# Optimization experiments

Measured on AMD Instinct MI355X. Metric: run time of the kernel, lower is better.

## Reference

```python
import jax, jax.numpy as jnp
import numpy as np

B = 32768
SEQ_LEN = 24
H = 64            # HIDDEN_DIM
SLOTS = 8         # MEMORY_SLOTS
VOCAB = 64        # VOCAB_SIZE


def setup_inputs() -> dict:
    key = jax.random.key(0)
    ks = jax.random.split(key, 8)
    seqs = jax.random.randint(ks[0], (B, SEQ_LEN), 0, VOCAB, dtype=jnp.int64)
    query_tok = jax.random.randint(ks[1], (B,), 0, VOCAB + 2, dtype=jnp.int64)
    embed = jax.random.normal(ks[2], (VOCAB + 2, H), dtype=jnp.float32) * 0.05
    gw1 = jax.random.normal(ks[3], (2 * H, 32), dtype=jnp.float32) / np.sqrt(2 * H)
    gb1 = jnp.zeros((32,), jnp.float32)
    gw2 = jax.random.normal(ks[4], (32, 1), dtype=jnp.float32) / np.sqrt(32)
    gb2 = jnp.zeros((1,), jnp.float32)
    rw1 = jax.random.normal(ks[5], (2 * H, H), dtype=jnp.float32) / np.sqrt(2 * H)
    rb1 = jnp.zeros((H,), jnp.float32)
    rw2 = jax.random.normal(ks[6], (H, VOCAB), dtype=jnp.float32) / np.sqrt(H)
    rb2 = jnp.zeros((VOCAB,), jnp.float32)
    return {"seqs": seqs, "query_tok": query_tok, "embed": embed,
            "gw1": gw1, "gb1": gb1, "gw2": gw2, "gb2": gb2,
            "rw1": rw1, "rb1": rb1, "rw2": rw2, "rb2": rb2}


def reference(seqs, query_tok, embed, gw1, gb1, gw2, gb2, rw1, rb1, rw2, rb2):
    Bb = seqs.shape[0]
    T = SEQ_LEN - 1  # model writes tokens 0..SEQ_LEN-2 into memory
    embs = embed[seqs[:, :T]]                     # [B, T, H]
    batch_idx = jnp.arange(Bb)

    def step(mem, xs):
        t, emb = xs                               # emb: [B, H]
        ctx = jnp.broadcast_to(emb[:, None, :], mem.shape)
        pair = jnp.concatenate([ctx, mem], axis=-1)        # [B, S, 2H]
        h = jax.nn.relu(pair @ gw1 + gb1)                  # [B, S, 32]
        score = jax.nn.sigmoid(h @ gw2 + gb2)[..., 0]      # [B, S]
        # while memory not full, fill slot t; otherwise evict argmax score
        idx = jnp.where(t < SLOTS, t, jnp.argmax(score, axis=1))
        mem = mem.at[batch_idx, idx].set(emb)
        return mem, None

    mem0 = jnp.zeros((Bb, SLOTS, H), embed.dtype)
    mem, _ = jax.lax.scan(step, mem0, (jnp.arange(T), jnp.swapaxes(embs, 0, 1)))

    summary = mem.mean(axis=1)                    # [B, H]  (memory is full: T > SLOTS)
    q = embed[query_tok]                          # [B, H]
    x = jnp.concatenate([q, summary], axis=-1)    # [B, 2H]
    logits = jax.nn.relu(x @ rw1 + rb1) @ rw2 + rb2   # [B, VOCAB]
    return logits
```

## Files before the change

kernel.cpp:

```cpp
#include <hip/hip_runtime.h>
#include <math.h>

typedef __attribute__((ext_vector_type(8))) _Float16 f16x8;
typedef __attribute__((ext_vector_type(4))) float f32x4;

#define TSTEPS 23

#define WSB_Z  0
#define WSB_B1 16384
#define WSB_W2 37888

__global__ __launch_bounds__(256) void pre_all(
    const float* __restrict__ embed, const float* __restrict__ gw1,
    const float* __restrict__ gb1, const float* __restrict__ gw2,
    const float* __restrict__ gb2, const float* __restrict__ rw1,
    const float* __restrict__ rb1, const float* __restrict__ rw2,
    char* __restrict__ wsc)
{
    __shared__ float sEmb[66 * 64];
    __shared__ float sW[128 * 64];
    __shared__ float sV[64 * 33];
    __shared__ float sU[4 * 32];
    __shared__ float sG[65];
    __shared__ float sRb1[64];

    const int tid = threadIdx.x;
    const int blk = blockIdx.x;

    if (blk < 16) {
        {
            const float4* es = (const float4*)embed;
            float4* ed = (float4*)sEmb;
            for (int i = tid; i < 1024; i += 256) ed[i] = es[i];
            const float4* gs = (const float4*)gw1;
            float4* gd = (float4*)sW;
            for (int i = tid; i < 1024; i += 256) gd[i] = gs[i];
            if (tid < 32) { sG[tid] = gb1[tid]; sG[32 + tid] = gw2[tid]; }
            if (tid == 64) sG[64] = gb2[0];
        }
        __syncthreads();
        #pragma unroll
        for (int i = 0; i < 8; ++i) {
            const int e = tid + i * 256;
            const int s = e >> 5, j = e & 31;
            float acc = 0.f;
            const float* er = sEmb + s * 64;
            #pragma unroll
            for (int k = 0; k < 64; ++k)
                acc = fmaf(er[k], sW[(64 + k) * 32 + j], acc);
            sV[s * 33 + j] = acc;
        }
        if (tid < 128) {
            const int cc = tid >> 5, j = tid & 31;
            const int c = blk * 4 + cc;
            float acc = 0.f;
            const float* er = sEmb + c * 64;
            #pragma unroll
            for (int k = 0; k < 64; ++k)
                acc = fmaf(er[k], sW[k * 32 + j], acc);
            sU[cc * 32 + j] = acc;
        }
        __syncthreads();
        const int cc = tid >> 6, s = tid & 63;
        const int c = blk * 4 + cc;
        double z = (double)sG[64];
        #pragma unroll
        for (int j = 0; j < 32; ++j) {
            const double a = (double)sU[cc * 32 + j] + (double)sV[s * 33 + j] + (double)sG[j];
            if (a > 0.0) z += a * (double)sG[32 + j];
        }
        ((float*)(wsc + WSB_Z))[c * 64 + s] = (float)(1.0 / (1.0 + exp(-z)));
    } else if (blk < 49) {
        {
            const float4* es = (const float4*)embed;
            float4* ed = (float4*)sEmb;
            for (int i = tid; i < 1056; i += 256) ed[i] = es[i];
            const float4* rs = (const float4*)rw1;
            float4* rd = (float4*)sW;
            for (int i = tid; i < 2048; i += 256) rd[i] = rs[i];
            if (tid < 64) sRb1[tid] = rb1[tid];
        }
        __syncthreads();
        const int e = (blk - 16) * 256 + tid;
        if (e < 8320) {
            const int n = e & 63, k = e >> 6;
            float acc;
            if (k < 64) {
                acc = 0.f;
                const float* er = sEmb + k * 64;
                #pragma unroll
                for (int m = 0; m < 64; ++m)
                    acc = fmaf(er[m], sW[(64 + m) * 64 + n], acc);
                acc *= 0.125f * 256.f;
            } else {
                const int t = k - 64;
                acc = sRb1[n];
                const float* er = sEmb + t * 64;
                #pragma unroll
                for (int m = 0; m < 64; ++m)
                    acc = fmaf(er[m], sW[m * 64 + n], acc);
                acc *= 256.f;
            }
            ((_Float16*)(wsc + WSB_B1))[n * 168 + k] = (_Float16)acc;
        }
    } else {
        _Float16* w2t = (_Float16*)(wsc + WSB_W2);
        for (int e = tid; e < 4096; e += 256) {
            const int n = e & 63, j = e >> 6;
            w2t[n * 72 + j] = (_Float16)rw2[j * 64 + n];
        }
        _Float16* b1 = (_Float16*)(wsc + WSB_B1);
        for (int e = tid; e < 2432; e += 256) {
            const int n = e / 38, k = 130 + (e - n * 38);
            b1[n * 168 + k] = (_Float16)0.f;
        }
    }
}

#define ROWS 128

__global__ __launch_bounds__(512, 2) void sm_main(
    const int* __restrict__ seqs, const int* __restrict__ qtok,
    const float* __restrict__ rb2, const char* __restrict__ wsc,
    float* __restrict__ out)
{
    __shared__ __align__(16) float     sZ[64 * 64];
    __shared__ __align__(16) _Float16  sB1[64 * 168];
    __shared__ __align__(16) _Float16  sA[128 * 168];
    __shared__ __align__(16) _Float16  sW2[64 * 72];
    __shared__ __align__(16) _Float16  sH[128 * 72];
    __shared__ float sRb2[64];

    const int tid = threadIdx.x;
    const int base = blockIdx.x * ROWS;

    unsigned pk[6];
    int qt = 0;
    if (tid < ROWS) {
        const int4* sq = (const int4*)(seqs + (size_t)(base + tid) * 24);
        #pragma unroll
        for (int i = 0; i < 6; ++i) {
            const int4 w4 = sq[i];
            pk[i] = (unsigned)w4.x | ((unsigned)w4.y << 8) |
                    ((unsigned)w4.z << 16) | ((unsigned)w4.w << 24);
        }
        qt = qtok[base + tid];
    }

    {
        const float4* zsrc = (const float4*)(wsc + WSB_Z);
        float4* zdst = (float4*)sZ;
        for (int i = tid; i < 1024; i += 512) zdst[i] = zsrc[i];
        const float4* b1s = (const float4*)(wsc + WSB_B1);
        float4* b1d = (float4*)sB1;
        for (int i = tid; i < 1344; i += 512) b1d[i] = b1s[i];
        const float4* w2s = (const float4*)(wsc + WSB_W2);
        float4* w2d = (float4*)sW2;
        for (int i = tid; i < 576; i += 512) w2d[i] = w2s[i];
        const float4 z4 = {0.f, 0.f, 0.f, 0.f};
        float4* ad = (float4*)sA;
        for (int i = tid; i < 2688; i += 512) ad[i] = z4;
        if (tid < 64) sRb2[tid] = rb2[tid];
    }
    __syncthreads();

    if (tid < ROWS) {
        unsigned lo = pk[0], hi = pk[1];
        #pragma unroll
        for (int t = 8; t < TSTEPS; ++t) {
            const int c = (int)((pk[t >> 2] >> ((t & 3) * 8)) & 255u);
            const float* zr = sZ + c * 64;
            float b = zr[lo & 63]; int am = 0; float z;
            z = zr[(lo >> 8) & 63];  if (z > b) { b = z; am = 1; }
            z = zr[(lo >> 16) & 63]; if (z > b) { b = z; am = 2; }
            z = zr[lo >> 24];        if (z > b) { b = z; am = 3; }
            z = zr[hi & 63];         if (z > b) { b = z; am = 4; }
            z = zr[(hi >> 8) & 63];  if (z > b) { b = z; am = 5; }
            z = zr[(hi >> 16) & 63]; if (z > b) { b = z; am = 6; }
            z = zr[hi >> 24];        if (z > b) { b = z; am = 7; }
            const unsigned cb = (unsigned)c;
            if (am < 4) { const int sh = am * 8; lo = (lo & ~(255u << sh)) | (cb << sh); }
            else        { const int sh = am * 8 - 32; hi = (hi & ~(255u << sh)) | (cb << sh); }
        }
        int t_[8] = { (int)(lo & 63), (int)((lo >> 8) & 63), (int)((lo >> 16) & 63), (int)(lo >> 24),
                      (int)(hi & 63), (int)((hi >> 8) & 63), (int)((hi >> 16) & 63), (int)(hi >> 24) };
        int tot[8] = {1, 1, 1, 1, 1, 1, 1, 1};
        #pragma unroll
        for (int i = 0; i < 8; ++i)
            #pragma unroll
            for (int j = i + 1; j < 8; ++j) {
                const int eq = (t_[i] == t_[j]);
                tot[i] += eq; tot[j] += eq;
            }
        _Float16* arow = sA + tid * 168;
        #pragma unroll
        for (int i = 0; i < 8; ++i) arow[t_[i]] = (_Float16)(float)tot[i];
        arow[64 + qt] = (_Float16)1.0f;
    }
    __syncthreads();

    const int lane = tid & 63;
    const int w = tid >> 6;
    const int c16 = lane & 15, g = lane >> 4;
    const int arow = w * 16 + c16;
    f32x4 a0 = {0.f, 0.f, 0.f, 0.f}, a1 = a0, a2 = a0, a3 = a0;
    #pragma unroll
    for (int ks = 0; ks < 5; ++ks) {
        const int ko = ks * 32 + g * 8;
        const f16x8 af = *(const f16x8*)&sA[arow * 168 + ko];
        const f16x8 b0 = *(const f16x8*)&sB1[(c16) * 168 + ko];
        const f16x8 b1 = *(const f16x8*)&sB1[(16 + c16) * 168 + ko];
        const f16x8 b2 = *(const f16x8*)&sB1[(32 + c16) * 168 + ko];
        const f16x8 b3 = *(const f16x8*)&sB1[(48 + c16) * 168 + ko];
        a0 = __builtin_amdgcn_mfma_f32_16x16x32_f16(af, b0, a0, 0, 0, 0);
        a1 = __builtin_amdgcn_mfma_f32_16x16x32_f16(af, b1, a1, 0, 0, 0);
        a2 = __builtin_amdgcn_mfma_f32_16x16x32_f16(af, b2, a2, 0, 0, 0);
        a3 = __builtin_amdgcn_mfma_f32_16x16x32_f16(af, b3, a3, 0, 0, 0);
    }
    {
        const int rbase = w * 16 + g * 4;
        #pragma unroll
        for (int j = 0; j < 4; ++j) {
            _Float16* hr = sH + (rbase + j) * 72;
            const float v0 = a0[j], v1 = a1[j], v2 = a2[j], v3 = a3[j];
            hr[c16]      = (_Float16)(v0 > 0.f ? v0 : 0.f);
            hr[16 + c16] = (_Float16)(v1 > 0.f ? v1 : 0.f);
            hr[32 + c16] = (_Float16)(v2 > 0.f ? v2 : 0.f);
            hr[48 + c16] = (_Float16)(v3 > 0.f ? v3 : 0.f);
        }
    }
    __syncthreads();

    f32x4 d0 = {0.f, 0.f, 0.f, 0.f}, d1 = d0, d2 = d0, d3 = d0;
    #pragma unroll
    for (int ks = 0; ks < 2; ++ks) {
        const int ko = ks * 32 + g * 8;
        const f16x8 af = *(const f16x8*)&sH[arow * 72 + ko];
        const f16x8 b0 = *(const f16x8*)&sW2[(c16) * 72 + ko];
        const f16x8 b1 = *(const f16x8*)&sW2[(16 + c16) * 72 + ko];
        const f16x8 b2 = *(const f16x8*)&sW2[(32 + c16) * 72 + ko];
        const f16x8 b3 = *(const f16x8*)&sW2[(48 + c16) * 72 + ko];
        d0 = __builtin_amdgcn_mfma_f32_16x16x32_f16(af, b0, d0, 0, 0, 0);
        d1 = __builtin_amdgcn_mfma_f32_16x16x32_f16(af, b1, d1, 0, 0, 0);
        d2 = __builtin_amdgcn_mfma_f32_16x16x32_f16(af, b2, d2, 0, 0, 0);
        d3 = __builtin_amdgcn_mfma_f32_16x16x32_f16(af, b3, d3, 0, 0, 0);
    }
    float* sOut = (float*)(void*)sA;
    {
        const int rbase = w * 16 + g * 4;
        #pragma unroll
        for (int j = 0; j < 4; ++j) {
            float* orow = sOut + (rbase + j) * 68;
            orow[c16]      = d0[j] * (1.f / 256.f) + sRb2[c16];
            orow[16 + c16] = d1[j] * (1.f / 256.f) + sRb2[16 + c16];
            orow[32 + c16] = d2[j] * (1.f / 256.f) + sRb2[32 + c16];
            orow[48 + c16] = d3[j] * (1.f / 256.f) + sRb2[48 + c16];
        }
    }
    __syncthreads();

    #pragma unroll
    for (int r2 = 0; r2 < 4; ++r2) {
        const int idx = r2 * 512 + tid;
        const int row = idx >> 4, c4 = idx & 15;
        *(float4*)(out + (size_t)(base + row) * 64 + c4 * 4) =
            *(const float4*)&sOut[row * 68 + c4 * 4];
    }
}

extern "C" void kernel_launch(void* const* d_in, const int* in_sizes, int n_in,
                              void* d_out, int out_size, void* d_ws, size_t ws_size,
                              hipStream_t stream)
{
    const int* seqs    = (const int*)d_in[0];
    const int* qtok    = (const int*)d_in[1];
    const float* embed = (const float*)d_in[2];
    const float* gw1   = (const float*)d_in[3];
    const float* gb1   = (const float*)d_in[4];
    const float* gw2   = (const float*)d_in[5];
    const float* gb2   = (const float*)d_in[6];
    const float* rw1   = (const float*)d_in[7];
    const float* rb1   = (const float*)d_in[8];
    const float* rw2   = (const float*)d_in[9];
    const float* rb2   = (const float*)d_in[10];
    char* wsc  = (char*)d_ws;
    float* out = (float*)d_out;
    const int B = in_sizes[1];

    pre_all<<<50, 256, 0, stream>>>(embed, gw1, gb1, gw2, gb2, rw1, rb1, rw2, wsc);
    sm_main<<<B / ROWS, 512, 0, stream>>>(seqs, qtok, rb2, wsc, out);
}
```

Baseline: 22.82 us.

## Fuse precompute and main kernels with an atomic flag handoff

Merges the weight-precompute kernel into the main kernel. The first 34 blocks do the precompute, write it to the workspace and bump an atomic counter, and every block spin-waits on that counter before loading the tables into shared memory. The goal is to remove one kernel launch and its inter-kernel gap. In exchange it adds a memset launch, a grid-wide spin wait that depends on the producer blocks being resident, and a serial dependency: all 256 blocks stall until the producer blocks finish.

```diff
diff --git a/kernel.cpp b/kernel.cpp
--- a/kernel.cpp
+++ b/kernel.cpp
@@ -5,134 +5,48 @@
 typedef __attribute__((ext_vector_type(4))) float f32x4;
 
 #define TSTEPS 23
-
-#define WSB_Z  0
-#define WSB_B1 16384
-#define WSB_W2 37888
-
-__global__ __launch_bounds__(256) void pre_all(
+#define ROWS 128
+#define NPROD 34
+
+#define WSB_Z    0
+#define WSB_B1   16384
+#define WSB_W2   37888
+#define WSB_FLAG 49152
+
+#define L_Z    0
+#define L_B1   16384
+#define L_W2   37888
+#define L_H    47104
+#define L_A    65536
+#define L_RB2  108544
+#define P_EMB  47104
+#define P_W    64000
+#define P_V    96768
+#define P_U    105216
+#define P_G    105728
+#define P_RB1  106240
+
+__global__ __launch_bounds__(512, 2) void sm_fused(
+    const int* __restrict__ seqs, const int* __restrict__ qtok,
     const float* __restrict__ embed, const float* __restrict__ gw1,
     const float* __restrict__ gb1, const float* __restrict__ gw2,
     const float* __restrict__ gb2, const float* __restrict__ rw1,
     const float* __restrict__ rb1, const float* __restrict__ rw2,
-    char* __restrict__ wsc)
+    const float* __restrict__ rb2,
+    char* __restrict__ wsc, float* __restrict__ out)
 {
-    __shared__ float sEmb[66 * 64];
-    __shared__ float sW[128 * 64];
-    __shared__ float sV[64 * 33];
-    __shared__ float sU[4 * 32];
-    __shared__ float sG[65];
-    __shared__ float sRb1[64];
+    __shared__ __align__(16) char smem[108800];
+    float*    sZ   = (float*)(smem + L_Z);
+    _Float16* sB1  = (_Float16*)(smem + L_B1);
+    _Float16* sW2  = (_Float16*)(smem + L_W2);
+    _Float16* sH   = (_Float16*)(smem + L_H);
+    _Float16* sA   = (_Float16*)(smem + L_A);
+    float*    sRb2 = (float*)(smem + L_RB2);
 
     const int tid = threadIdx.x;
     const int blk = blockIdx.x;
-
-    if (blk < 16) {
-        {
-            const float4* es = (const float4*)embed;
-            float4* ed = (float4*)sEmb;
-            for (int i = tid; i < 1024; i += 256) ed[i] = es[i];
-            const float4* gs = (const float4*)gw1;
-            float4* gd = (float4*)sW;
-            for (int i = tid; i < 1024; i += 256) gd[i] = gs[i];
-            if (tid < 32) { sG[tid] = gb1[tid]; sG[32 + tid] = gw2[tid]; }
-            if (tid == 64) sG[64] = gb2[0];
-        }
-        __syncthreads();
-        #pragma unroll
-        for (int i = 0; i < 8; ++i) {
-            const int e = tid + i * 256;
-            const int s = e >> 5, j = e & 31;
-            float acc = 0.f;
-            const float* er = sEmb + s * 64;
-            #pragma unroll
-            for (int k = 0; k < 64; ++k)
-                acc = fmaf(er[k], sW[(64 + k) * 32 + j], acc);
-            sV[s * 33 + j] = acc;
-        }
-        if (tid < 128) {
-            const int cc = tid >> 5, j = tid & 31;
-            const int c = blk * 4 + cc;
-            float acc = 0.f;
-            const float* er = sEmb + c * 64;
-            #pragma unroll
-            for (int k = 0; k < 64; ++k)
-                acc = fmaf(er[k], sW[k * 32 + j], acc);
-            sU[cc * 32 + j] = acc;
-        }
-        __syncthreads();
-        const int cc = tid >> 6, s = tid & 63;
-        const int c = blk * 4 + cc;
-        double z = (double)sG[64];
-        #pragma unroll
-        for (int j = 0; j < 32; ++j) {
-            const double a = (double)sU[cc * 32 + j] + (double)sV[s * 33 + j] + (double)sG[j];
-            if (a > 0.0) z += a * (double)sG[32 + j];
-        }
-        ((float*)(wsc + WSB_Z))[c * 64 + s] = (float)(1.0 / (1.0 + exp(-z)));
-    } else if (blk < 49) {
-        {
-            const float4* es = (const float4*)embed;
-            float4* ed = (float4*)sEmb;
-            for (int i = tid; i < 1056; i += 256) ed[i] = es[i];
-            const float4* rs = (const float4*)rw1;
-            float4* rd = (float4*)sW;
-            for (int i = tid; i < 2048; i += 256) rd[i] = rs[i];
-            if (tid < 64) sRb1[tid] = rb1[tid];
-        }
-        __syncthreads();
-        const int e = (blk - 16) * 256 + tid;
-        if (e < 8320) {
-            const int n = e & 63, k = e >> 6;
-            float acc;
-            if (k < 64) {
-                acc = 0.f;
-                const float* er = sEmb + k * 64;
-                #pragma unroll
-                for (int m = 0; m < 64; ++m)
-                    acc = fmaf(er[m], sW[(64 + m) * 64 + n], acc);
-                acc *= 0.125f * 256.f;
-            } else {
-                const int t = k - 64;
-                acc = sRb1[n];
-                const float* er = sEmb + t * 64;
-                #pragma unroll
-                for (int m = 0; m < 64; ++m)
-                    acc = fmaf(er[m], sW[m * 64 + n], acc);
-                acc *= 256.f;
-            }
-            ((_Float16*)(wsc + WSB_B1))[n * 168 + k] = (_Float16)acc;
-        }
-    } else {
-        _Float16* w2t = (_Float16*)(wsc + WSB_W2);
-        for (int e = tid; e < 4096; e += 256) {
-            const int n = e & 63, j = e >> 6;
-            w2t[n * 72 + j] = (_Float16)rw2[j * 64 + n];
-        }
-        _Float16* b1 = (_Float16*)(wsc + WSB_B1);
-        for (int e = tid; e < 2432; e += 256) {
-            const int n = e / 38, k = 130 + (e - n * 38);
-            b1[n * 168 + k] = (_Float16)0.f;
-        }
-    }
-}
-
-#define ROWS 128
-
-__global__ __launch_bounds__(512, 2) void sm_main(
-    const int* __restrict__ seqs, const int* __restrict__ qtok,
-    const float* __restrict__ rb2, const char* __restrict__ wsc,
-    float* __restrict__ out)
-{
-    __shared__ __align__(16) float     sZ[64 * 64];
-    __shared__ __align__(16) _Float16  sB1[64 * 168];
-    __shared__ __align__(16) _Float16  sA[128 * 168];
-    __shared__ __align__(16) _Float16  sW2[64 * 72];
-    __shared__ __align__(16) _Float16  sH[128 * 72];
-    __shared__ float sRb2[64];
-
-    const int tid = threadIdx.x;
-    const int base = blockIdx.x * ROWS;
+    const int base = blk * ROWS;
+    unsigned* flag = (unsigned*)(wsc + WSB_FLAG);
 
     unsigned pk[6];
     int qt = 0;
@@ -146,21 +60,129 @@
         }
         qt = qtok[base + tid];
     }
+    float rb2v = 0.f;
+    if (tid < 64) rb2v = rb2[tid];
+
+    if (blk < NPROD) {
+        float* pEmb = (float*)(smem + P_EMB);
+        float* pW   = (float*)(smem + P_W);
+        if (blk < 16) {
+            float* pV = (float*)(smem + P_V);
+            float* pU = (float*)(smem + P_U);
+            float* pG = (float*)(smem + P_G);
+            {
+                const float4* es = (const float4*)embed;
+                float4* ed = (float4*)pEmb;
+                for (int i = tid; i < 1024; i += 512) ed[i] = es[i];
+                const float4* gs = (const float4*)gw1;
+                float4* gd = (float4*)pW;
+                for (int i = tid; i < 1024; i += 512) gd[i] = gs[i];
+                if (tid < 32) { pG[tid] = gb1[tid]; pG[32 + tid] = gw2[tid]; }
+                if (tid == 64) pG[64] = gb2[0];
+            }
+            __syncthreads();
+            #pragma unroll
+            for (int i = 0; i < 4; ++i) {
+                const int e = tid + i * 512;
+                const int s = e >> 5, j = e & 31;
+                float acc = 0.f;
+                const float* er = pEmb + s * 64;
+                #pragma unroll
+                for (int k = 0; k < 64; ++k)
+                    acc = fmaf(er[k], pW[(64 + k) * 32 + j], acc);
+                pV[s * 33 + j] = acc;
+            }
+            if (tid < 128) {
+                const int cc = tid >> 5, j = tid & 31;
+                const int c = blk * 4 + cc;
+                float acc = 0.f;
+                const float* er = pEmb + c * 64;
+                #pragma unroll
+                for (int k = 0; k < 64; ++k)
+                    acc = fmaf(er[k], pW[k * 32 + j], acc);
+                pU[cc * 32 + j] = acc;
+            }
+            __syncthreads();
+            if (tid < 256) {
+                const int cc = tid >> 6, s = tid & 63;
+                const int c = blk * 4 + cc;
+                double z = (double)pG[64];
+                #pragma unroll
+                for (int j = 0; j < 32; ++j) {
+                    const double a = (double)pU[cc * 32 + j] + (double)pV[s * 33 + j] + (double)pG[j];
+                    if (a > 0.0) z += a * (double)pG[32 + j];
+                }
+                ((float*)(wsc + WSB_Z))[c * 64 + s] = (float)(1.0 / (1.0 + exp(-z)));
+            }
+        } else if (blk < 33) {
+            float* pRb1 = (float*)(smem + P_RB1);
+            {
+                const float4* es = (const float4*)embed;
+                float4* ed = (float4*)pEmb;
+                for (int i = tid; i < 1056; i += 512) ed[i] = es[i];
+                const float4* rs = (const float4*)rw1;
+                float4* rd = (float4*)pW;
+                for (int i = tid; i < 2048; i += 512) rd[i] = rs[i];
+                if (tid < 64) pRb1[tid] = rb1[tid];
+            }
+            __syncthreads();
+            const int e = (blk - 16) * 512 + tid;
+            if (e < 8320) {
+                const int n = e & 63, k = e >> 6;
+                float acc;
+                if (k < 64) {
+                    acc = 0.f;
+                    const float* er = pEmb + k * 64;
+                    #pragma unroll
+                    for (int m = 0; m < 64; ++m)
+                        acc = fmaf(er[m], pW[(64 + m) * 64 + n], acc);
+                    acc *= 0.125f * 256.f;
+                } else {
+                    const int t = k - 64;
+                    acc = pRb1[n];
+                    const float* er = pEmb + t * 64;
+                    #pragma unroll
+                    for (int m = 0; m < 64; ++m)
+                        acc = fmaf(er[m], pW[m * 64 + n], acc);
+                    acc *= 256.f;
+                }
+                ((_Float16*)(wsc + WSB_B1))[n * 168 + k] = (_Float16)acc;
+            }
+        } else {
+            _Float16* w2t = (_Float16*)(wsc + WSB_W2);
+            for (int e = tid; e < 4096; e += 512) {
+                const int n = e & 63, j = e >> 6;
+                w2t[n * 72 + j] = (_Float16)rw2[j * 64 + n];
+            }
+            _Float16* b1 = (_Float16*)(wsc + WSB_B1);
+            for (int e = tid; e < 2432; e += 512) {
+                const int n = e / 38, k = 130 + (e - n * 38);
+                b1[n * 168 + k] = (_Float16)0.f;
+            }
+        }
+        __syncthreads();
+        __threadfence();
+        if (tid == 0)
+            __hip_atomic_fetch_add(flag, 1u, __ATOMIC_RELEASE, __HIP_MEMORY_SCOPE_AGENT);
+    }
+
+    if (tid == 0) {
+        while (__hip_atomic_load(flag, __ATOMIC_ACQUIRE, __HIP_MEMORY_SCOPE_AGENT) < (unsigned)NPROD)
+            __builtin_amdgcn_s_sleep(8);
+    }
+    __syncthreads();
 
     {
-        const float4* zsrc = (const float4*)(wsc + WSB_Z);
-        float4* zdst = (float4*)sZ;
-        for (int i = tid; i < 1024; i += 512) zdst[i] = zsrc[i];
-        const float4* b1s = (const float4*)(wsc + WSB_B1);
-        float4* b1d = (float4*)sB1;
-        for (int i = tid; i < 1344; i += 512) b1d[i] = b1s[i];
-        const float4* w2s = (const float4*)(wsc + WSB_W2);
-        float4* w2d = (float4*)sW2;
-        for (int i = tid; i < 576; i += 512) w2d[i] = w2s[i];
+        const unsigned long long* zsrc = (const unsigned long long*)(wsc + WSB_Z);
+        unsigned long long* zdst = (unsigned long long*)sZ;
+        #pragma unroll
+        for (int i = 0; i < 4; ++i)
+            zdst[tid + i * 512] =
+                __hip_atomic_load(&zsrc[tid + i * 512], __ATOMIC_RELAXED, __HIP_MEMORY_SCOPE_AGENT);
         const float4 z4 = {0.f, 0.f, 0.f, 0.f};
         float4* ad = (float4*)sA;
         for (int i = tid; i < 2688; i += 512) ad[i] = z4;
-        if (tid < 64) sRb2[tid] = rb2[tid];
+        if (tid < 64) sRb2[tid] = rb2v;
     }
     __syncthreads();
 
@@ -196,6 +218,16 @@
         #pragma unroll
         for (int i = 0; i < 8; ++i) arow[t_[i]] = (_Float16)(float)tot[i];
         arow[64 + qt] = (_Float16)1.0f;
+    } else {
+        const int t2 = tid - 128;
+        const unsigned long long* b1s = (const unsigned long long*)(wsc + WSB_B1);
+        unsigned long long* b1d = (unsigned long long*)sB1;
+        for (int i = t2; i < 2688; i += 384)
+            b1d[i] = __hip_atomic_load(&b1s[i], __ATOMIC_RELAXED, __HIP_MEMORY_SCOPE_AGENT);
+        const unsigned long long* w2s = (const unsigned long long*)(wsc + WSB_W2);
+        unsigned long long* w2d = (unsigned long long*)sW2;
+        for (int i = t2; i < 1152; i += 384)
+            w2d[i] = __hip_atomic_load(&w2s[i], __ATOMIC_RELAXED, __HIP_MEMORY_SCOPE_AGENT);
     }
     __syncthreads();
 
@@ -287,6 +319,7 @@
     float* out = (float*)d_out;
     const int B = in_sizes[1];
 
-    pre_all<<<50, 256, 0, stream>>>(embed, gw1, gb1, gw2, gb2, rw1, rb1, rw2, wsc);
-    sm_main<<<B / ROWS, 512, 0, stream>>>(seqs, qtok, rb2, wsc, out);
+    hipMemsetAsync(wsc + WSB_FLAG, 0, 4, stream);
+    sm_fused<<<B / ROWS, 512, 0, stream>>>(seqs, qtok, embed, gw1, gb1, gw2, gb2,
+                                           rw1, rb1, rw2, rb2, wsc, out);
 }
```

New measurement: 78.71 us. +245.0%, slower.

## Move gate score table build from prekernel into main kernel per block

Applied to the files above, without the earlier changes.

The prekernel now only computes the U and V projections of the embedding through the gate's first layer. Each main-kernel block rebuilds the full 64x64 sigmoid score table in shared memory from U and V, using double-precision math. The B1/W2 weight loads are staged in registers so they overlap with that computation, and the score table gets a padded stride of 65 to cut bank conflicts. The aim is to shorten the serial prekernel, at the cost of every one of the 256 blocks redundantly running a 4096x32 double-precision loop, which is slow on the GPU.

```diff
diff --git a/kernel.cpp b/kernel.cpp
--- a/kernel.cpp
+++ b/kernel.cpp
@@ -5,23 +5,20 @@
 typedef __attribute__((ext_vector_type(4))) float f32x4;
 
 #define TSTEPS 23
-
-#define WSB_Z  0
-#define WSB_B1 16384
-#define WSB_W2 37888
-
-__global__ __launch_bounds__(256) void pre_all(
+#define ROWS 128
+
+#define WSB_B1 0
+#define WSB_W2 21504
+#define WSB_U  30720
+#define WSB_V  38912
+
+__global__ __launch_bounds__(256) void pre_lite(
     const float* __restrict__ embed, const float* __restrict__ gw1,
-    const float* __restrict__ gb1, const float* __restrict__ gw2,
-    const float* __restrict__ gb2, const float* __restrict__ rw1,
-    const float* __restrict__ rb1, const float* __restrict__ rw2,
-    char* __restrict__ wsc)
+    const float* __restrict__ rw1, const float* __restrict__ rb1,
+    const float* __restrict__ rw2, char* __restrict__ wsc)
 {
     __shared__ float sEmb[66 * 64];
     __shared__ float sW[128 * 64];
-    __shared__ float sV[64 * 33];
-    __shared__ float sU[4 * 32];
-    __shared__ float sG[65];
     __shared__ float sRb1[64];
 
     const int tid = threadIdx.x;
@@ -31,45 +28,22 @@
         {
             const float4* es = (const float4*)embed;
             float4* ed = (float4*)sEmb;
-            for (int i = tid; i < 1024; i += 256) ed[i] = es[i];
+            for (int i = tid; i < 1056; i += 256) ed[i] = es[i];
             const float4* gs = (const float4*)gw1;
             float4* gd = (float4*)sW;
             for (int i = tid; i < 1024; i += 256) gd[i] = gs[i];
-            if (tid < 32) { sG[tid] = gb1[tid]; sG[32 + tid] = gw2[tid]; }
-            if (tid == 64) sG[64] = gb2[0];
         }
         __syncthreads();
-        #pragma unroll
-        for (int i = 0; i < 8; ++i) {
-            const int e = tid + i * 256;
-            const int s = e >> 5, j = e & 31;
-            float acc = 0.f;
-            const float* er = sEmb + s * 64;
-            #pragma unroll
-            for (int k = 0; k < 64; ++k)
-                acc = fmaf(er[k], sW[(64 + k) * 32 + j], acc);
-            sV[s * 33 + j] = acc;
-        }
-        if (tid < 128) {
-            const int cc = tid >> 5, j = tid & 31;
-            const int c = blk * 4 + cc;
-            float acc = 0.f;
-            const float* er = sEmb + c * 64;
-            #pragma unroll
-            for (int k = 0; k < 64; ++k)
-                acc = fmaf(er[k], sW[k * 32 + j], acc);
-            sU[cc * 32 + j] = acc;
-        }
-        __syncthreads();
-        const int cc = tid >> 6, s = tid & 63;
-        const int c = blk * 4 + cc;
-        double z = (double)sG[64];
-        #pragma unroll
-        for (int j = 0; j < 32; ++j) {
-            const double a = (double)sU[cc * 32 + j] + (double)sV[s * 33 + j] + (double)sG[j];
-            if (a > 0.0) z += a * (double)sG[32 + j];
-        }
-        ((float*)(wsc + WSB_Z))[c * 64 + s] = (float)(1.0 / (1.0 + exp(-z)));
+        const int e = blk * 256 + tid;
+        const int row = (e >> 5) & 63, j = e & 31;
+        const int ofs = (e < 2048) ? 0 : 64;
+        float acc = 0.f;
+        const float* er = sEmb + row * 64;
+        #pragma unroll
+        for (int k = 0; k < 64; ++k)
+            acc = fmaf(er[k], sW[(ofs + k) * 32 + j], acc);
+        float* dst = (float*)(wsc + ((e < 2048) ? WSB_U : WSB_V));
+        dst[e & 2047] = acc;
     } else if (blk < 49) {
         {
             const float4* es = (const float4*)embed;
@@ -117,19 +91,32 @@
     }
 }
 
-#define ROWS 128
+#define L_A    0
+#define L_B1   43008
+#define L_W2   64512
+#define L_Z    73728
+#define L_H    90368
+#define L_U    90368
+#define L_V    98816
+#define L_G    107264
+#define L_RB2  108800
 
 __global__ __launch_bounds__(512, 2) void sm_main(
     const int* __restrict__ seqs, const int* __restrict__ qtok,
-    const float* __restrict__ rb2, const char* __restrict__ wsc,
-    float* __restrict__ out)
+    const float* __restrict__ gb1, const float* __restrict__ gw2,
+    const float* __restrict__ gb2, const float* __restrict__ rb2,
+    const char* __restrict__ wsc, float* __restrict__ out)
 {
-    __shared__ __align__(16) float     sZ[64 * 64];
-    __shared__ __align__(16) _Float16  sB1[64 * 168];
-    __shared__ __align__(16) _Float16  sA[128 * 168];
-    __shared__ __align__(16) _Float16  sW2[64 * 72];
-    __shared__ __align__(16) _Float16  sH[128 * 72];
-    __shared__ float sRb2[64];
+    __shared__ __align__(16) char smem[109056];
+    _Float16* sA   = (_Float16*)(smem + L_A);
+    _Float16* sB1  = (_Float16*)(smem + L_B1);
+    _Float16* sW2  = (_Float16*)(smem + L_W2);
+    float*    sZ   = (float*)(smem + L_Z);
+    _Float16* sH   = (_Float16*)(smem + L_H);
+    float*    sU   = (float*)(smem + L_U);
+    float*    sV   = (float*)(smem + L_V);
+    float*    sG   = (float*)(smem + L_G);
+    float*    sRb2 = (float*)(smem + L_RB2);
 
     const int tid = threadIdx.x;
     const int base = blockIdx.x * ROWS;
@@ -148,19 +135,57 @@
     }
 
     {
-        const float4* zsrc = (const float4*)(wsc + WSB_Z);
-        float4* zdst = (float4*)sZ;
-        for (int i = tid; i < 1024; i += 512) zdst[i] = zsrc[i];
-        const float4* b1s = (const float4*)(wsc + WSB_B1);
-        float4* b1d = (float4*)sB1;
-        for (int i = tid; i < 1344; i += 512) b1d[i] = b1s[i];
-        const float4* w2s = (const float4*)(wsc + WSB_W2);
-        float4* w2d = (float4*)sW2;
-        for (int i = tid; i < 576; i += 512) w2d[i] = w2s[i];
+        const float* u = (const float*)(wsc + WSB_U);
+        const float* v = (const float*)(wsc + WSB_V);
+        #pragma unroll
+        for (int i = 0; i < 4; ++i) {
+            const int e = tid + i * 512;
+            sU[(e >> 5) * 33 + (e & 31)] = u[e];
+            sV[(e >> 5) * 33 + (e & 31)] = v[e];
+        }
+        if (tid < 32) { sG[tid] = gb1[tid]; sG[32 + tid] = gw2[tid]; }
+        if (tid == 64) sG[64] = gb2[0];
+        if (tid < 64) sRb2[tid] = rb2[tid];
         const float4 z4 = {0.f, 0.f, 0.f, 0.f};
         float4* ad = (float4*)sA;
         for (int i = tid; i < 2688; i += 512) ad[i] = z4;
-        if (tid < 64) sRb2[tid] = rb2[tid];
+    }
+    __syncthreads();
+
+    float4 stg[4];
+    {
+        const float4* b1s = (const float4*)(wsc + WSB_B1);
+        const float4* w2s = (const float4*)(wsc + WSB_W2);
+        #pragma unroll
+        for (int m = 0; m < 4; ++m) {
+            const int flat = tid + m * 512;
+            if (flat < 1344)      stg[m] = b1s[flat];
+            else if (flat < 1920) stg[m] = w2s[flat - 1344];
+        }
+    }
+    #pragma unroll
+    for (int i = 0; i < 8; ++i) {
+        const int idx = tid + i * 512;
+        const int c = idx >> 6, s = idx & 63;
+        double z = (double)sG[64];
+        #pragma unroll
+        for (int j = 0; j < 32; ++j) {
+            const double a = (double)sU[c * 33 + j] + (double)sV[s * 33 + j] + (double)sG[j];
+            if (a > 0.0) z += a * (double)sG[32 + j];
+        }
+        sZ[c * 65 + s] = (float)(1.0 / (1.0 + exp(-z)));
+    }
+    __syncthreads();
+
+    {
+        float4* b1d = (float4*)sB1;
+        float4* w2d = (float4*)sW2;
+        #pragma unroll
+        for (int m = 0; m < 4; ++m) {
+            const int flat = tid + m * 512;
+            if (flat < 1344)      b1d[flat] = stg[m];
+            else if (flat < 1920) w2d[flat - 1344] = stg[m];
+        }
     }
     __syncthreads();
 
@@ -169,7 +194,7 @@
         #pragma unroll
         for (int t = 8; t < TSTEPS; ++t) {
             const int c = (int)((pk[t >> 2] >> ((t & 3) * 8)) & 255u);
-            const float* zr = sZ + c * 64;
+            const float* zr = sZ + c * 65;
             float b = zr[lo & 63]; int am = 0; float z;
             z = zr[(lo >> 8) & 63];  if (z > b) { b = z; am = 1; }
             z = zr[(lo >> 16) & 63]; if (z > b) { b = z; am = 2; }
@@ -287,6 +312,6 @@
     float* out = (float*)d_out;
     const int B = in_sizes[1];
 
-    pre_all<<<50, 256, 0, stream>>>(embed, gw1, gb1, gw2, gb2, rw1, rb1, rw2, wsc);
-    sm_main<<<B / ROWS, 512, 0, stream>>>(seqs, qtok, rb2, wsc, out);
+    pre_lite<<<50, 256, 0, stream>>>(embed, gw1, rw1, rb1, rw2, wsc);
+    sm_main<<<B / ROWS, 512, 0, stream>>>(seqs, qtok, gb1, gw2, gb2, rb2, wsc, out);
 }
```

New measurement: 43.38 us. +90.1%, slower.

## Build sparse MFMA A-operand in registers instead of zeroed LDS matrix

Applied to the files above, without the earlier changes.

Drops the 128x168 fp16 A matrix in shared memory, which had to be zero-filled and then scattered into. Each row now stores only a compact packed record (slot ids, counts, query token), and every lane builds its 8-element MFMA A fragment in registers with compare/select logic. This cuts LDS footprint and the zero-fill traffic, and the launch bounds are raised to 4 blocks per CU to exploit the smaller footprint. The cost is extra ALU work per k-step and possible register pressure at the higher occupancy target. The output staging buffer now aliases the start of shared memory (the sZ/sB1 region) rather than the removed A buffer.

```diff
diff --git a/kernel.cpp b/kernel.cpp
--- a/kernel.cpp
+++ b/kernel.cpp
@@ -5,6 +5,7 @@
 typedef __attribute__((ext_vector_type(4))) float f32x4;
 
 #define TSTEPS 23
+#define ROWS 128
 
 #define WSB_Z  0
 #define WSB_B1 16384
@@ -61,15 +62,17 @@
             sU[cc * 32 + j] = acc;
         }
         __syncthreads();
-        const int cc = tid >> 6, s = tid & 63;
-        const int c = blk * 4 + cc;
-        double z = (double)sG[64];
-        #pragma unroll
-        for (int j = 0; j < 32; ++j) {
-            const double a = (double)sU[cc * 32 + j] + (double)sV[s * 33 + j] + (double)sG[j];
-            if (a > 0.0) z += a * (double)sG[32 + j];
-        }
-        ((float*)(wsc + WSB_Z))[c * 64 + s] = (float)(1.0 / (1.0 + exp(-z)));
+        {
+            const int cc = tid >> 6, s = tid & 63;
+            const int c = blk * 4 + cc;
+            double z = (double)sG[64];
+            #pragma unroll
+            for (int j = 0; j < 32; ++j) {
+                const double a = (double)sU[cc * 32 + j] + (double)sV[s * 33 + j] + (double)sG[j];
+                if (a > 0.0) z += a * (double)sG[32 + j];
+            }
+            ((float*)(wsc + WSB_Z))[c * 64 + s] = (float)(1.0 / (1.0 + exp(-z)));
+        }
     } else if (blk < 49) {
         {
             const float4* es = (const float4*)embed;
@@ -117,19 +120,56 @@
     }
 }
 
-#define ROWS 128
-
-__global__ __launch_bounds__(512, 2) void sm_main(
+__device__ __forceinline__ f16x8 build_slot_win(const unsigned* s, const unsigned* hb, int ko)
+{
+    unsigned w0 = 0, w1 = 0, w2 = 0, w3 = 0;
+    #pragma unroll
+    for (int i = 0; i < 8; ++i) {
+        const unsigned d = s[i] - (unsigned)ko;
+        const unsigned val = (d < 8u) ? (hb[i] << ((d & 1u) * 16)) : 0u;
+        const unsigned q = d >> 1;
+        w0 |= (q == 0u) ? val : 0u;
+        w1 |= (q == 1u) ? val : 0u;
+        w2 |= (q == 2u) ? val : 0u;
+        w3 |= (q == 3u) ? val : 0u;
+    }
+    union { unsigned u[4]; f16x8 v; } r;
+    r.u[0] = w0; r.u[1] = w1; r.u[2] = w2; r.u[3] = w3;
+    return r.v;
+}
+
+__device__ __forceinline__ f16x8 build_q_win(int kq, int ko)
+{
+    const unsigned d = (unsigned)(kq - ko);
+    const unsigned val = (d < 8u) ? (0x3C00u << ((d & 1u) * 16)) : 0u;
+    const unsigned q = d >> 1;
+    union { unsigned u[4]; f16x8 v; } r;
+    r.u[0] = (q == 0u) ? val : 0u;
+    r.u[1] = (q == 1u) ? val : 0u;
+    r.u[2] = (q == 2u) ? val : 0u;
+    r.u[3] = (q == 3u) ? val : 0u;
+    return r.v;
+}
+
+#define L_Z    0
+#define L_B1   16384
+#define L_W2   37888
+#define L_H    47104
+#define L_ROW  65536
+#define L_RB2  67584
+
+__global__ __launch_bounds__(512, 4) void sm_main(
     const int* __restrict__ seqs, const int* __restrict__ qtok,
     const float* __restrict__ rb2, const char* __restrict__ wsc,
     float* __restrict__ out)
 {
-    __shared__ __align__(16) float     sZ[64 * 64];
-    __shared__ __align__(16) _Float16  sB1[64 * 168];
-    __shared__ __align__(16) _Float16  sA[128 * 168];
-    __shared__ __align__(16) _Float16  sW2[64 * 72];
-    __shared__ __align__(16) _Float16  sH[128 * 72];
-    __shared__ float sRb2[64];
+    __shared__ __align__(16) char smem[67840];
+    float*    sZ   = (float*)(smem + L_Z);
+    _Float16* sB1  = (_Float16*)(smem + L_B1);
+    _Float16* sW2  = (_Float16*)(smem + L_W2);
+    _Float16* sH   = (_Float16*)(smem + L_H);
+    uint4*    sRow = (uint4*)(smem + L_ROW);
+    float*    sRb2 = (float*)(smem + L_RB2);
 
     const int tid = threadIdx.x;
     const int base = blockIdx.x * ROWS;
@@ -157,9 +197,6 @@
         const float4* w2s = (const float4*)(wsc + WSB_W2);
         float4* w2d = (float4*)sW2;
         for (int i = tid; i < 576; i += 512) w2d[i] = w2s[i];
-        const float4 z4 = {0.f, 0.f, 0.f, 0.f};
-        float4* ad = (float4*)sA;
-        for (int i = tid; i < 2688; i += 512) ad[i] = z4;
         if (tid < 64) sRb2[tid] = rb2[tid];
     }
     __syncthreads();
@@ -192,10 +229,10 @@
                 const int eq = (t_[i] == t_[j]);
                 tot[i] += eq; tot[j] += eq;
             }
-        _Float16* arow = sA + tid * 168;
-        #pragma unroll
-        for (int i = 0; i < 8; ++i) arow[t_[i]] = (_Float16)(float)tot[i];
-        arow[64 + qt] = (_Float16)1.0f;
+        unsigned tp = 0;
+        #pragma unroll
+        for (int i = 0; i < 8; ++i) tp |= (unsigned)tot[i] << (4 * i);
+        sRow[tid] = make_uint4(lo & 0x3F3F3F3Fu, hi & 0x3F3F3F3Fu, tp, (unsigned)qt);
     }
     __syncthreads();
 
@@ -203,11 +240,30 @@
     const int w = tid >> 6;
     const int c16 = lane & 15, g = lane >> 4;
     const int arow = w * 16 + c16;
+
+    unsigned sl[8], hb[8];
+    int kq;
+    {
+        const uint4 ri = sRow[arow];
+        sl[0] = ri.x & 63u; sl[1] = (ri.x >> 8) & 63u;
+        sl[2] = (ri.x >> 16) & 63u; sl[3] = ri.x >> 24;
+        sl[4] = ri.y & 63u; sl[5] = (ri.y >> 8) & 63u;
+        sl[6] = (ri.y >> 16) & 63u; sl[7] = ri.y >> 24;
+        #pragma unroll
+        for (int i = 0; i < 8; ++i) {
+            const unsigned tot = (ri.z >> (4 * i)) & 15u;
+            union { _Float16 h; unsigned short b; } cv;
+            cv.h = (_Float16)(float)tot;
+            hb[i] = (unsigned)cv.b;
+        }
+        kq = 64 + (int)ri.w;
+    }
+
     f32x4 a0 = {0.f, 0.f, 0.f, 0.f}, a1 = a0, a2 = a0, a3 = a0;
     #pragma unroll
     for (int ks = 0; ks < 5; ++ks) {
         const int ko = ks * 32 + g * 8;
-        const f16x8 af = *(const f16x8*)&sA[arow * 168 + ko];
+        const f16x8 af = (ks < 2) ? build_slot_win(sl, hb, ko) : build_q_win(kq, ko);
         const f16x8 b0 = *(const f16x8*)&sB1[(c16) * 168 + ko];
         const f16x8 b1 = *(const f16x8*)&sB1[(16 + c16) * 168 + ko];
         const f16x8 b2 = *(const f16x8*)&sB1[(32 + c16) * 168 + ko];
@@ -245,7 +301,7 @@
         d2 = __builtin_amdgcn_mfma_f32_16x16x32_f16(af, b2, d2, 0, 0, 0);
         d3 = __builtin_amdgcn_mfma_f32_16x16x32_f16(af, b3, d3, 0, 0, 0);
     }
-    float* sOut = (float*)(void*)sA;
+    float* sOut = (float*)(void*)smem;
     {
         const int rbase = w * 16 + g * 4;
         #pragma unroll
```

Result: slower. 23.72 us (+3.9%).
